# Performance work log

Measured on AMD Instinct MI355X. Metric: run time of the kernel, lower is better.

Reference implementation:

```python
import jax, jax.numpy as jnp
import numpy as np

N_NODES = 100000
N_EDGES = 1600000
IN_DIM = 128
OUT_DIM = 32
NUM_HEADS = 4


def setup_inputs() -> dict:
    key = jax.random.key(0)
    k1, k2, k3, k4, k5, k6 = jax.random.split(key, 6)
    feat = jax.random.normal(k1, (N_NODES, IN_DIM), dtype=jnp.float32)
    # xavier-uniform-ish scales
    fc_w = jax.random.normal(k2, (OUT_DIM * NUM_HEADS, IN_DIM), dtype=jnp.float32) * (1.0 / np.sqrt(IN_DIM))
    attn_src = jax.random.normal(k3, (1, NUM_HEADS, OUT_DIM), dtype=jnp.float32) * 0.1
    attn_dst = jax.random.normal(k4, (1, NUM_HEADS, OUT_DIM), dtype=jnp.float32) * 0.1
    src = jax.random.randint(k5, (N_EDGES,), 0, N_NODES, dtype=jnp.int64)
    dst = jax.random.randint(k6, (N_EDGES,), 0, N_NODES, dtype=jnp.int64)
    return {"feat": feat, "fc_w": fc_w, "attn_src": attn_src, "attn_dst": attn_dst, "src": src, "dst": dst}


def reference(feat, fc_w, attn_src, attn_dst, src, dst):
    N = feat.shape[0]
    # fc: [N, H*D] -> [N, H, D]
    h = (feat @ fc_w.T).reshape(N, NUM_HEADS, OUT_DIM)
    # per-node attention logits [N, H]
    e_src = jnp.sum(h * attn_src, axis=-1)
    e_dst = jnp.sum(h * attn_dst, axis=-1)
    # per-edge logits, LeakyReLU(0.2)  [E, H]
    e = e_src[src] + e_dst[dst]
    e = jnp.where(e > 0, e, 0.2 * e)
    # edge softmax over incoming edges of each dst node
    m = jax.ops.segment_max(e, dst, num_segments=N)          # [N, H], -inf for empty
    a = jnp.exp(e - m[dst])                                  # [E, H]
    s = jax.ops.segment_sum(a, dst, num_segments=N)          # [N, H]
    a = a / jnp.where(s[dst] > 0, s[dst], 1.0)
    # weighted scatter-sum aggregation: u_mul_e + sum
    msg = h[src] * a[:, :, None]                             # [E, H, D]
    out = jax.ops.segment_sum(msg, dst, num_segments=N)      # [N, H, D]
    h_out = out.reshape(N, NUM_HEADS * OUT_DIM)
    # residual: in_dim == out_dim*num_heads -> identity residual
    return h_out + feat
```

## Files before the change

### kernel.cpp

```cpp
#include <hip/hip_runtime.h>

#define HD 128
#define NHEADS 4
#define MBLK 128
#define APITCH 136

#define CHUNK_SHIFT 8
#define MAXCH 512
#define CLCAP 4352
#define PT_EDGES 2048
#define SUB_SHIFT 6
#define SUBN 64
#define CAP 48

#define H8_SCALE   15.875f
#define H8_INVSCALE 0.062992126f

typedef __attribute__((ext_vector_type(8))) short bf16x8;
typedef __attribute__((ext_vector_type(4))) float f32x4;

__device__ __forceinline__ unsigned short f2bf(float x) {
    union { float f; unsigned u; } a; a.f = x;
    unsigned r = a.u + 0x7fffu + ((a.u >> 16) & 1u);
    return (unsigned short)(r >> 16);
}

__global__ __launch_bounds__(256, 2) void gemm_part(
    const float* __restrict__ feat, const float* __restrict__ fc_w,
    const float* __restrict__ attn_src, const float* __restrict__ attn_dst,
    const int* __restrict__ src, const int* __restrict__ dst,
    signed char* __restrict__ h8, float* __restrict__ e_src, float* __restrict__ e_dst,
    int* __restrict__ cursor, unsigned int* __restrict__ clist,
    int2* __restrict__ spillP, int* __restrict__ nspillP,
    int N, int E, int epb, int nchunks, int spillPCap)
{
    __shared__ unsigned short As[MBLK * APITCH];
    __shared__ unsigned short Bs[HD * APITCH];
    const int tid = threadIdx.x;
    const int row0 = blockIdx.x * MBLK;

    {
        int* lcnt = (int*)As;
        int* gbase = lcnt + MAXCH;
        unsigned short* rnk = (unsigned short*)(gbase + MAXCH);
        const int ebase0 = blockIdx.x * epb;
        int eend = ebase0 + epb; if (eend > E) eend = E;
        for (int b0 = ebase0; b0 < eend; b0 += PT_EDGES) {
            int bend = b0 + PT_EDGES; if (bend > eend) bend = eend;
            for (int i = tid; i < MAXCH; i += 256) lcnt[i] = 0;
            __syncthreads();
#pragma unroll
            for (int k = 0; k < PT_EDGES / 256; k++) {
                int idx = tid + k * 256;
                int e = b0 + idx;
                if (e < bend) {
                    int d = dst[e];
                    rnk[idx] = (unsigned short)atomicAdd(&lcnt[d >> CHUNK_SHIFT], 1);
                }
            }
            __syncthreads();
            for (int c = tid; c < nchunks; c += 256) {
                int cnt = lcnt[c];
                gbase[c] = cnt ? atomicAdd(&cursor[c], cnt) : 0;
            }
            __syncthreads();
#pragma unroll
            for (int k = 0; k < PT_EDGES / 256; k++) {
                int idx = tid + k * 256;
                int e = b0 + idx;
                if (e < bend) {
                    int d = dst[e], s = src[e];
                    int c = d >> CHUNK_SHIFT;
                    int pos = gbase[c] + (int)rnk[idx];
                    if (pos < CLCAP && s < (1 << 24)) {
                        clist[(size_t)c * CLCAP + pos] =
                            ((unsigned)(d & (CHUNK_SHIFT == 8 ? 255 : 255)) << 24) | (unsigned)s;
                    } else {
                        int kk = atomicAdd(nspillP, 1);
                        if (kk < spillPCap) spillP[kk] = make_int2(d, s);
                    }
                }
            }
            __syncthreads();
        }
    }
    __syncthreads();

    for (int i = tid; i < 128 * 32; i += 256) {
        int o = i >> 5, j = i & 31;
        float4 v = ((const float4*)fc_w)[i];
        ushort4 u; u.x = f2bf(v.x); u.y = f2bf(v.y); u.z = f2bf(v.z); u.w = f2bf(v.w);
        *(ushort4*)&Bs[o * APITCH + j * 4] = u;
    }
    for (int i = tid; i < MBLK * 32; i += 256) {
        int r = i >> 5, j = i & 31;
        int rowg = row0 + r;
        float4 v = make_float4(0.f, 0.f, 0.f, 0.f);
        if (rowg < N) {
            v = ((const float4*)feat)[(size_t)rowg * 32 + j];
        }
        ushort4 u; u.x = f2bf(v.x); u.y = f2bf(v.y); u.z = f2bf(v.z); u.w = f2bf(v.w);
        *(ushort4*)&As[r * APITCH + j * 4] = u;
    }
    __syncthreads();

    const int w = tid >> 6, lane = tid & 63, quad = lane >> 4, lr = lane & 15;
    f32x4 acc[2][8];
#pragma unroll
    for (int rt = 0; rt < 2; rt++)
#pragma unroll
        for (int ct = 0; ct < 8; ct++) acc[rt][ct] = (f32x4){0.f, 0.f, 0.f, 0.f};

#pragma unroll
    for (int ks = 0; ks < 4; ks++) {
        const int k0 = ks * 32 + quad * 8;
        bf16x8 a0 = *(const bf16x8*)&As[(w * 32 + lr) * APITCH + k0];
        bf16x8 a1 = *(const bf16x8*)&As[(w * 32 + 16 + lr) * APITCH + k0];
        bf16x8 bf[8];
#pragma unroll
        for (int ct = 0; ct < 8; ct++)
            bf[ct] = *(const bf16x8*)&Bs[(ct * 16 + lr) * APITCH + k0];
#pragma unroll
        for (int ct = 0; ct < 8; ct++) {
            acc[0][ct] = __builtin_amdgcn_mfma_f32_16x16x32_bf16(a0, bf[ct], acc[0][ct], 0, 0, 0);
            acc[1][ct] = __builtin_amdgcn_mfma_f32_16x16x32_bf16(a1, bf[ct], acc[1][ct], 0, 0, 0);
        }
    }

#pragma unroll
    for (int rt = 0; rt < 2; rt++) {
#pragma unroll
        for (int ct = 0; ct < 8; ct++) {
            int col = ct * 16 + lr;
#pragma unroll
            for (int reg = 0; reg < 4; reg++) {
                int row = row0 + w * 32 + rt * 16 + quad * 4 + reg;
                if (row < N) {
                    float v = acc[rt][ct][reg];
                    v = fminf(fmaxf(v, -8.f), 8.f);
                    int q = (int)rintf(v * H8_SCALE);
                    h8[(size_t)row * 128 + col] = (signed char)q;
                }
            }
        }
    }

    float as_v[8], ad_v[8];
#pragma unroll
    for (int ct = 0; ct < 8; ct++) {
        as_v[ct] = attn_src[ct * 16 + lr];
        ad_v[ct] = attn_dst[ct * 16 + lr];
    }
#pragma unroll
    for (int rt = 0; rt < 2; rt++) {
#pragma unroll
        for (int reg = 0; reg < 4; reg++) {
            int row = row0 + w * 32 + rt * 16 + quad * 4 + reg;
            float ps[4], pd[4];
#pragma unroll
            for (int hd = 0; hd < 4; hd++) {
                ps[hd] = acc[rt][2 * hd][reg] * as_v[2 * hd] + acc[rt][2 * hd + 1][reg] * as_v[2 * hd + 1];
                pd[hd] = acc[rt][2 * hd][reg] * ad_v[2 * hd] + acc[rt][2 * hd + 1][reg] * ad_v[2 * hd + 1];
            }
#pragma unroll
            for (int off = 1; off < 16; off <<= 1) {
#pragma unroll
                for (int hd = 0; hd < 4; hd++) {
                    ps[hd] += __shfl_xor(ps[hd], off);
                    pd[hd] += __shfl_xor(pd[hd], off);
                }
            }
            if (lr == 0 && row < N) {
                *(float4*)&e_src[(size_t)row * 4] = make_float4(ps[0], ps[1], ps[2], ps[3]);
                *(float4*)&e_dst[(size_t)row * 4] = make_float4(pd[0], pd[1], pd[2], pd[3]);
            }
        }
    }
}

__global__ __launch_bounds__(512) void agg_chunk(
    const unsigned int* __restrict__ clist, const int* __restrict__ cursor,
    const int2* __restrict__ spillP, const int* __restrict__ nspillP,
    const signed char* __restrict__ h8,
    const float* __restrict__ e_src, const float* __restrict__ e_dst,
    const float* __restrict__ feat, float* __restrict__ out,
    int2* __restrict__ spillB, int* __restrict__ nspillB,
    int N, int spillPCap, int spillBCap)
{
    __shared__ int bucket[SUBN][CAP];
    __shared__ int lcnt[SUBN];
    const int c = blockIdx.x;
    const int tid = threadIdx.x;
    const int nodebase = c << SUB_SHIFT;
    const int sub = c & ((1 << (CHUNK_SHIFT - SUB_SHIFT)) - 1);

    if (tid < SUBN) lcnt[tid] = 0;
    __syncthreads();

    const int chunkC = c >> (CHUNK_SHIFT - SUB_SHIFT);
    int cnt = cursor[chunkC]; if (cnt > CLCAP) cnt = CLCAP;
    const unsigned int* base = clist + (size_t)chunkC * CLCAP;
    for (int i = tid; i < cnt; i += 512) {
        unsigned int p = base[i];
        int dl = (int)(p >> 24);
        if ((dl >> SUB_SHIFT) == sub) {
            int ln = dl & (SUBN - 1);
            int pos = atomicAdd(&lcnt[ln], 1);
            if (pos < CAP) bucket[ln][pos] = (int)(p & 0xFFFFFFu);
            else { int kk = atomicAdd(nspillB, 1); if (kk < spillBCap) spillB[kk] = make_int2(nodebase + ln, (int)(p & 0xFFFFFFu)); }
        }
    }
    int nsp = *nspillP; if (nsp > spillPCap) nsp = spillPCap;
    for (int i = tid; i < nsp; i += 512) {
        int2 p = spillP[i];
        if ((p.x >> SUB_SHIFT) == c) {
            int ln = p.x - nodebase;
            int pos = atomicAdd(&lcnt[ln], 1);
            if (pos < CAP) bucket[ln][pos] = p.y;
            else { int kk = atomicAdd(nspillB, 1); if (kk < spillBCap) spillB[kk] = p; }
        }
    }
    __syncthreads();

    const int lane  = tid & 63;
    const int wid   = tid >> 6;
    const int grp8  = lane >> 3;
    const int q     = lane & 7;
    const int head  = q >> 1;

    const int ln = wid * 8 + grp8;
    const int n = nodebase + ln;
    const bool active = (n < N);
    const int deg = active ? lcnt[ln] : 0;
    int md = deg;
    md = max(md, __shfl_xor(md, 8));
    md = max(md, __shfl_xor(md, 16));
    md = max(md, __shfl_xor(md, 32));
    if (md == 0) {
        if (active) {
            const float4* f = (const float4*)(feat + (size_t)n * HD) + q * 4;
            float4* o = (float4*)(out + (size_t)n * HD) + q * 4;
#pragma unroll
            for (int k = 0; k < 4; k++) o[k] = f[k];
        }
        return;
    }
    const float ed = active ? e_dst[(size_t)n * 4 + head] : 0.f;
    const int fdeg = deg < CAP ? deg : CAP;
    const int mdc = md < CAP ? md : CAP;

    f32x4 a0 = (f32x4){0.f, 0.f, 0.f, 0.f};
    f32x4 a1 = (f32x4){0.f, 0.f, 0.f, 0.f};
    f32x4 a2 = (f32x4){0.f, 0.f, 0.f, 0.f};
    f32x4 a3 = (f32x4){0.f, 0.f, 0.f, 0.f};
    float s_l = 0.f;
#pragma unroll 4
    for (int j = 0; j < mdc; ++j) {
        float ev = 0.f; int si = 0;
        if (j < fdeg) {
            si = bucket[ln][j];
            float v = e_src[(size_t)si * 4 + head] + ed;
            v = v > 0.f ? v : 0.2f * v;
            ev = __expf(v);
        }
        s_l += ev;
        const float evs = ev * H8_INVSCALE;
        uint4 hv = *(const uint4*)&h8[(size_t)si * 128 + q * 16];
        a0.x += evs * (float)(int)(signed char)(hv.x);
        a0.y += evs * (float)(int)(signed char)(hv.x >> 8);
        a0.z += evs * (float)(int)(signed char)(hv.x >> 16);
        a0.w += evs * (float)(int)(signed char)(hv.x >> 24);
        a1.x += evs * (float)(int)(signed char)(hv.y);
        a1.y += evs * (float)(int)(signed char)(hv.y >> 8);
        a1.z += evs * (float)(int)(signed char)(hv.y >> 16);
        a1.w += evs * (float)(int)(signed char)(hv.y >> 24);
        a2.x += evs * (float)(int)(signed char)(hv.z);
        a2.y += evs * (float)(int)(signed char)(hv.z >> 8);
        a2.z += evs * (float)(int)(signed char)(hv.z >> 16);
        a2.w += evs * (float)(int)(signed char)(hv.z >> 24);
        a3.x += evs * (float)(int)(signed char)(hv.w);
        a3.y += evs * (float)(int)(signed char)(hv.w >> 8);
        a3.z += evs * (float)(int)(signed char)(hv.w >> 16);
        a3.w += evs * (float)(int)(signed char)(hv.w >> 24);
    }
    if (__any(deg > CAP)) {
        int ns = *nspillB; if (ns > spillBCap) ns = spillBCap;
        for (int k = 0; k < ns; ++k) {
            int2 p = spillB[k];
            if (active && deg > CAP && p.x == n) {
                int si = p.y;
                float v = e_src[(size_t)si * 4 + head] + ed;
                v = v > 0.f ? v : 0.2f * v;
                float ev = __expf(v);
                s_l += ev;
                const float evs = ev * H8_INVSCALE;
                uint4 hv = *(const uint4*)&h8[(size_t)si * 128 + q * 16];
                a0.x += evs * (float)(int)(signed char)(hv.x);
                a0.y += evs * (float)(int)(signed char)(hv.x >> 8);
                a0.z += evs * (float)(int)(signed char)(hv.x >> 16);
                a0.w += evs * (float)(int)(signed char)(hv.x >> 24);
                a1.x += evs * (float)(int)(signed char)(hv.y);
                a1.y += evs * (float)(int)(signed char)(hv.y >> 8);
                a1.z += evs * (float)(int)(signed char)(hv.y >> 16);
                a1.w += evs * (float)(int)(signed char)(hv.y >> 24);
                a2.x += evs * (float)(int)(signed char)(hv.z);
                a2.y += evs * (float)(int)(signed char)(hv.z >> 8);
                a2.z += evs * (float)(int)(signed char)(hv.z >> 16);
                a2.w += evs * (float)(int)(signed char)(hv.z >> 24);
                a3.x += evs * (float)(int)(signed char)(hv.w);
                a3.y += evs * (float)(int)(signed char)(hv.w >> 8);
                a3.z += evs * (float)(int)(signed char)(hv.w >> 16);
                a3.w += evs * (float)(int)(signed char)(hv.w >> 24);
            }
        }
    }
    if (active) {
        const float inv = (deg > 0) ? (1.0f / s_l) : 0.f;
        const float4* f = (const float4*)(feat + (size_t)n * HD) + q * 4;
        float4* o = (float4*)(out + (size_t)n * HD) + q * 4;
        float4 c0 = f[0], c1 = f[1], c2 = f[2], c3 = f[3];
        c0.x += a0.x * inv; c0.y += a0.y * inv; c0.z += a0.z * inv; c0.w += a0.w * inv;
        c1.x += a1.x * inv; c1.y += a1.y * inv; c1.z += a1.z * inv; c1.w += a1.w * inv;
        c2.x += a2.x * inv; c2.y += a2.y * inv; c2.z += a2.z * inv; c2.w += a2.w * inv;
        c3.x += a3.x * inv; c3.y += a3.y * inv; c3.z += a3.z * inv; c3.w += a3.w * inv;
        o[0] = c0; o[1] = c1; o[2] = c2; o[3] = c3;
    }
}

extern "C" void kernel_launch(void* const* d_in, const int* in_sizes, int n_in,
                              void* d_out, int out_size, void* d_ws, size_t ws_size,
                              hipStream_t stream) {
    const float* feat     = (const float*)d_in[0];
    const float* fc_w     = (const float*)d_in[1];
    const float* attn_src = (const float*)d_in[2];
    const float* attn_dst = (const float*)d_in[3];
    const int*   src      = (const int*)d_in[4];
    const int*   dst      = (const int*)d_in[5];
    const int N = in_sizes[0] / HD;
    const int E = in_sizes[4];
    float* out = (float*)d_out;

    const int nchunks = (N + 255) >> CHUNK_SHIFT;
    const int nsub    = (N + SUBN - 1) >> SUB_SHIFT;
    const int spillPCap = E / 8;
    const int spillBCap = E / 8;

    signed char* h8 = (signed char*)d_ws;
    float* e_src  = (float*)(h8 + (size_t)N * HD);
    float* e_dst  = e_src + (size_t)N * NHEADS;
    int* cursor   = (int*)(e_dst + (size_t)N * NHEADS);
    int* nspillP  = cursor + nchunks;
    int* nspillB  = nspillP + 1;
    int hdr = nchunks + 2;
    hdr = (hdr + 1) & ~1;
    unsigned int* clist = (unsigned int*)(cursor + hdr);
    size_t clistLen = (size_t)nchunks * CLCAP;
    clistLen = (clistLen + 1) & ~(size_t)1;
    int2* spillP  = (int2*)(clist + clistLen);
    int2* spillB  = spillP + spillPCap;

    const int G = (N + MBLK - 1) / MBLK;
    const int epb = ((E + G - 1) / G + PT_EDGES - 1) / PT_EDGES * PT_EDGES;

    hipMemsetAsync(cursor, 0, (size_t)(nchunks + 2) * sizeof(int), stream);
    gemm_part<<<G, 256, 0, stream>>>(feat, fc_w, attn_src, attn_dst, src, dst,
                                     h8, e_src, e_dst, cursor, clist, spillP, nspillP,
                                     N, E, epb, nchunks, spillPCap);
    agg_chunk<<<nsub, 512, 0, stream>>>(clist, cursor, spillP, nspillP,
                                        h8, e_src, e_dst, feat, out,
                                        spillB, nspillB, N, spillPCap, spillBCap);
}
```

Measured before the change: 228.6 us.

## Aggregate whole 256-node chunks per block and partition edges into larger slabs

The aggregation kernel now processes an entire 256-node chunk per 1024-thread block, two passes of 128 nodes each. Before, four 64-node sub-blocks each re-read the full chunk edge list and filtered it, so this removes that redundant clist scanning. The edge partition step now hands out fixed 8192-edge slabs in a grid-stride loop instead of per-block ranges, which reduces global cursor atomics per slab. In exchange the aggregation grid shrinks to about 391 large blocks using about 49KB of LDS each, which can lower occupancy and load balance, and the longer slabs lengthen the partition phase inside the GEMM kernel.

```diff
diff --git a/kernel.cpp b/kernel.cpp
--- a/kernel.cpp
+++ b/kernel.cpp
@@ -6,11 +6,10 @@
 #define APITCH 136
 
 #define CHUNK_SHIFT 8
+#define CHUNK_NODES 256
 #define MAXCH 512
 #define CLCAP 4352
-#define PT_EDGES 2048
-#define SUB_SHIFT 6
-#define SUBN 64
+#define PT_EDGES 8192
 #define CAP 48
 
 #define H8_SCALE   15.875f
@@ -32,7 +31,7 @@
     signed char* __restrict__ h8, float* __restrict__ e_src, float* __restrict__ e_dst,
     int* __restrict__ cursor, unsigned int* __restrict__ clist,
     int2* __restrict__ spillP, int* __restrict__ nspillP,
-    int N, int E, int epb, int nchunks, int spillPCap)
+    int N, int E, int npart, int nchunks, int spillPCap)
 {
     __shared__ unsigned short As[MBLK * APITCH];
     __shared__ unsigned short Bs[HD * APITCH];
@@ -43,13 +42,12 @@
         int* lcnt = (int*)As;
         int* gbase = lcnt + MAXCH;
         unsigned short* rnk = (unsigned short*)(gbase + MAXCH);
-        const int ebase0 = blockIdx.x * epb;
-        int eend = ebase0 + epb; if (eend > E) eend = E;
-        for (int b0 = ebase0; b0 < eend; b0 += PT_EDGES) {
-            int bend = b0 + PT_EDGES; if (bend > eend) bend = eend;
+        for (int sb = blockIdx.x; sb < npart; sb += gridDim.x) {
+            const int b0 = sb * PT_EDGES;
+            int bend = b0 + PT_EDGES; if (bend > E) bend = E;
             for (int i = tid; i < MAXCH; i += 256) lcnt[i] = 0;
             __syncthreads();
-#pragma unroll
+#pragma unroll 4
             for (int k = 0; k < PT_EDGES / 256; k++) {
                 int idx = tid + k * 256;
                 int e = b0 + idx;
@@ -64,7 +62,7 @@
                 gbase[c] = cnt ? atomicAdd(&cursor[c], cnt) : 0;
             }
             __syncthreads();
-#pragma unroll
+#pragma unroll 4
             for (int k = 0; k < PT_EDGES / 256; k++) {
                 int idx = tid + k * 256;
                 int e = b0 + idx;
@@ -73,8 +71,7 @@
                     int c = d >> CHUNK_SHIFT;
                     int pos = gbase[c] + (int)rnk[idx];
                     if (pos < CLCAP && s < (1 << 24)) {
-                        clist[(size_t)c * CLCAP + pos] =
-                            ((unsigned)(d & (CHUNK_SHIFT == 8 ? 255 : 255)) << 24) | (unsigned)s;
+                        clist[(size_t)c * CLCAP + pos] = ((unsigned)(d & 255) << 24) | (unsigned)s;
                     } else {
                         int kk = atomicAdd(nspillP, 1);
                         if (kk < spillPCap) spillP[kk] = make_int2(d, s);
@@ -178,7 +175,7 @@
     }
 }
 
-__global__ __launch_bounds__(512) void agg_chunk(
+__global__ __launch_bounds__(1024) void agg_chunk(
     const unsigned int* __restrict__ clist, const int* __restrict__ cursor,
     const int2* __restrict__ spillP, const int* __restrict__ nspillP,
     const signed char* __restrict__ h8,
@@ -187,33 +184,28 @@
     int2* __restrict__ spillB, int* __restrict__ nspillB,
     int N, int spillPCap, int spillBCap)
 {
-    __shared__ int bucket[SUBN][CAP];
-    __shared__ int lcnt[SUBN];
+    __shared__ int bucket[CHUNK_NODES][CAP];
+    __shared__ int lcnt[CHUNK_NODES];
     const int c = blockIdx.x;
     const int tid = threadIdx.x;
-    const int nodebase = c << SUB_SHIFT;
-    const int sub = c & ((1 << (CHUNK_SHIFT - SUB_SHIFT)) - 1);
-
-    if (tid < SUBN) lcnt[tid] = 0;
+    const int nodebase = c << CHUNK_SHIFT;
+
+    if (tid < CHUNK_NODES) lcnt[tid] = 0;
     __syncthreads();
 
-    const int chunkC = c >> (CHUNK_SHIFT - SUB_SHIFT);
-    int cnt = cursor[chunkC]; if (cnt > CLCAP) cnt = CLCAP;
-    const unsigned int* base = clist + (size_t)chunkC * CLCAP;
-    for (int i = tid; i < cnt; i += 512) {
+    int cnt = cursor[c]; if (cnt > CLCAP) cnt = CLCAP;
+    const unsigned int* base = clist + (size_t)c * CLCAP;
+    for (int i = tid; i < cnt; i += 1024) {
         unsigned int p = base[i];
-        int dl = (int)(p >> 24);
-        if ((dl >> SUB_SHIFT) == sub) {
-            int ln = dl & (SUBN - 1);
-            int pos = atomicAdd(&lcnt[ln], 1);
-            if (pos < CAP) bucket[ln][pos] = (int)(p & 0xFFFFFFu);
-            else { int kk = atomicAdd(nspillB, 1); if (kk < spillBCap) spillB[kk] = make_int2(nodebase + ln, (int)(p & 0xFFFFFFu)); }
-        }
+        int ln = (int)(p >> 24);
+        int pos = atomicAdd(&lcnt[ln], 1);
+        if (pos < CAP) bucket[ln][pos] = (int)(p & 0xFFFFFFu);
+        else { int kk = atomicAdd(nspillB, 1); if (kk < spillBCap) spillB[kk] = make_int2(nodebase + ln, (int)(p & 0xFFFFFFu)); }
     }
     int nsp = *nspillP; if (nsp > spillPCap) nsp = spillPCap;
-    for (int i = tid; i < nsp; i += 512) {
+    for (int i = tid; i < nsp; i += 1024) {
         int2 p = spillP[i];
-        if ((p.x >> SUB_SHIFT) == c) {
+        if ((p.x >> CHUNK_SHIFT) == c) {
             int ln = p.x - nodebase;
             int pos = atomicAdd(&lcnt[ln], 1);
             if (pos < CAP) bucket[ln][pos] = p.y;
@@ -228,102 +220,105 @@
     const int q     = lane & 7;
     const int head  = q >> 1;
 
-    const int ln = wid * 8 + grp8;
-    const int n = nodebase + ln;
-    const bool active = (n < N);
-    const int deg = active ? lcnt[ln] : 0;
-    int md = deg;
-    md = max(md, __shfl_xor(md, 8));
-    md = max(md, __shfl_xor(md, 16));
-    md = max(md, __shfl_xor(md, 32));
-    if (md == 0) {
+#pragma unroll
+    for (int pass = 0; pass < 2; pass++) {
+        const int ln = pass * 128 + wid * 8 + grp8;
+        const int n = nodebase + ln;
+        const bool active = (n < N);
+        const int deg = active ? lcnt[ln] : 0;
+        int md = deg;
+        md = max(md, __shfl_xor(md, 8));
+        md = max(md, __shfl_xor(md, 16));
+        md = max(md, __shfl_xor(md, 32));
+        if (md == 0) {
+            if (active) {
+                const float4* f = (const float4*)(feat + (size_t)n * HD) + q * 4;
+                float4* o = (float4*)(out + (size_t)n * HD) + q * 4;
+#pragma unroll
+                for (int k = 0; k < 4; k++) o[k] = f[k];
+            }
+            continue;
+        }
+        const float ed = active ? e_dst[(size_t)n * 4 + head] : 0.f;
+        const int fdeg = deg < CAP ? deg : CAP;
+        const int mdc = md < CAP ? md : CAP;
+
+        f32x4 a0 = (f32x4){0.f, 0.f, 0.f, 0.f};
+        f32x4 a1 = (f32x4){0.f, 0.f, 0.f, 0.f};
+        f32x4 a2 = (f32x4){0.f, 0.f, 0.f, 0.f};
+        f32x4 a3 = (f32x4){0.f, 0.f, 0.f, 0.f};
+        float s_l = 0.f;
+#pragma unroll 4
+        for (int j = 0; j < mdc; ++j) {
+            float ev = 0.f; int si = 0;
+            if (j < fdeg) {
+                si = bucket[ln][j];
+                float v = e_src[(size_t)si * 4 + head] + ed;
+                v = v > 0.f ? v : 0.2f * v;
+                ev = __expf(v);
+            }
+            s_l += ev;
+            const float evs = ev * H8_INVSCALE;
+            uint4 hv = *(const uint4*)&h8[(size_t)si * 128 + q * 16];
+            a0.x += evs * (float)(int)(signed char)(hv.x);
+            a0.y += evs * (float)(int)(signed char)(hv.x >> 8);
+            a0.z += evs * (float)(int)(signed char)(hv.x >> 16);
+            a0.w += evs * (float)(int)(signed char)(hv.x >> 24);
+            a1.x += evs * (float)(int)(signed char)(hv.y);
+            a1.y += evs * (float)(int)(signed char)(hv.y >> 8);
+            a1.z += evs * (float)(int)(signed char)(hv.y >> 16);
+            a1.w += evs * (float)(int)(signed char)(hv.y >> 24);
+            a2.x += evs * (float)(int)(signed char)(hv.z);
+            a2.y += evs * (float)(int)(signed char)(hv.z >> 8);
+            a2.z += evs * (float)(int)(signed char)(hv.z >> 16);
+            a2.w += evs * (float)(int)(signed char)(hv.z >> 24);
+            a3.x += evs * (float)(int)(signed char)(hv.w);
+            a3.y += evs * (float)(int)(signed char)(hv.w >> 8);
+            a3.z += evs * (float)(int)(signed char)(hv.w >> 16);
+            a3.w += evs * (float)(int)(signed char)(hv.w >> 24);
+        }
+        if (__any(deg > CAP)) {
+            int ns = *nspillB; if (ns > spillBCap) ns = spillBCap;
+            for (int k = 0; k < ns; ++k) {
+                int2 p = spillB[k];
+                if (active && deg > CAP && p.x == n) {
+                    int si = p.y;
+                    float v = e_src[(size_t)si * 4 + head] + ed;
+                    v = v > 0.f ? v : 0.2f * v;
+                    float ev = __expf(v);
+                    s_l += ev;
+                    const float evs = ev * H8_INVSCALE;
+                    uint4 hv = *(const uint4*)&h8[(size_t)si * 128 + q * 16];
+                    a0.x += evs * (float)(int)(signed char)(hv.x);
+                    a0.y += evs * (float)(int)(signed char)(hv.x >> 8);
+                    a0.z += evs * (float)(int)(signed char)(hv.x >> 16);
+                    a0.w += evs * (float)(int)(signed char)(hv.x >> 24);
+                    a1.x += evs * (float)(int)(signed char)(hv.y);
+                    a1.y += evs * (float)(int)(signed char)(hv.y >> 8);
+                    a1.z += evs * (float)(int)(signed char)(hv.y >> 16);
+                    a1.w += evs * (float)(int)(signed char)(hv.y >> 24);
+                    a2.x += evs * (float)(int)(signed char)(hv.z);
+                    a2.y += evs * (float)(int)(signed char)(hv.z >> 8);
+                    a2.z += evs * (float)(int)(signed char)(hv.z >> 16);
+                    a2.w += evs * (float)(int)(signed char)(hv.z >> 24);
+                    a3.x += evs * (float)(int)(signed char)(hv.w);
+                    a3.y += evs * (float)(int)(signed char)(hv.w >> 8);
+                    a3.z += evs * (float)(int)(signed char)(hv.w >> 16);
+                    a3.w += evs * (float)(int)(signed char)(hv.w >> 24);
+                }
+            }
+        }
         if (active) {
+            const float inv = (deg > 0) ? (1.0f / s_l) : 0.f;
             const float4* f = (const float4*)(feat + (size_t)n * HD) + q * 4;
             float4* o = (float4*)(out + (size_t)n * HD) + q * 4;
-#pragma unroll
-            for (int k = 0; k < 4; k++) o[k] = f[k];
-        }
-        return;
-    }
-    const float ed = active ? e_dst[(size_t)n * 4 + head] : 0.f;
-    const int fdeg = deg < CAP ? deg : CAP;
-    const int mdc = md < CAP ? md : CAP;
-
-    f32x4 a0 = (f32x4){0.f, 0.f, 0.f, 0.f};
-    f32x4 a1 = (f32x4){0.f, 0.f, 0.f, 0.f};
-    f32x4 a2 = (f32x4){0.f, 0.f, 0.f, 0.f};
-    f32x4 a3 = (f32x4){0.f, 0.f, 0.f, 0.f};
-    float s_l = 0.f;
-#pragma unroll 4
-    for (int j = 0; j < mdc; ++j) {
-        float ev = 0.f; int si = 0;
-        if (j < fdeg) {
-            si = bucket[ln][j];
-            float v = e_src[(size_t)si * 4 + head] + ed;
-            v = v > 0.f ? v : 0.2f * v;
-            ev = __expf(v);
-        }
-        s_l += ev;
-        const float evs = ev * H8_INVSCALE;
-        uint4 hv = *(const uint4*)&h8[(size_t)si * 128 + q * 16];
-        a0.x += evs * (float)(int)(signed char)(hv.x);
-        a0.y += evs * (float)(int)(signed char)(hv.x >> 8);
-        a0.z += evs * (float)(int)(signed char)(hv.x >> 16);
-        a0.w += evs * (float)(int)(signed char)(hv.x >> 24);
-        a1.x += evs * (float)(int)(signed char)(hv.y);
-        a1.y += evs * (float)(int)(signed char)(hv.y >> 8);
-        a1.z += evs * (float)(int)(signed char)(hv.y >> 16);
-        a1.w += evs * (float)(int)(signed char)(hv.y >> 24);
-        a2.x += evs * (float)(int)(signed char)(hv.z);
-        a2.y += evs * (float)(int)(signed char)(hv.z >> 8);
-        a2.z += evs * (float)(int)(signed char)(hv.z >> 16);
-        a2.w += evs * (float)(int)(signed char)(hv.z >> 24);
-        a3.x += evs * (float)(int)(signed char)(hv.w);
-        a3.y += evs * (float)(int)(signed char)(hv.w >> 8);
-        a3.z += evs * (float)(int)(signed char)(hv.w >> 16);
-        a3.w += evs * (float)(int)(signed char)(hv.w >> 24);
-    }
-    if (__any(deg > CAP)) {
-        int ns = *nspillB; if (ns > spillBCap) ns = spillBCap;
-        for (int k = 0; k < ns; ++k) {
-            int2 p = spillB[k];
-            if (active && deg > CAP && p.x == n) {
-                int si = p.y;
-                float v = e_src[(size_t)si * 4 + head] + ed;
-                v = v > 0.f ? v : 0.2f * v;
-                float ev = __expf(v);
-                s_l += ev;
-                const float evs = ev * H8_INVSCALE;
-                uint4 hv = *(const uint4*)&h8[(size_t)si * 128 + q * 16];
-                a0.x += evs * (float)(int)(signed char)(hv.x);
-                a0.y += evs * (float)(int)(signed char)(hv.x >> 8);
-                a0.z += evs * (float)(int)(signed char)(hv.x >> 16);
-                a0.w += evs * (float)(int)(signed char)(hv.x >> 24);
-                a1.x += evs * (float)(int)(signed char)(hv.y);
-                a1.y += evs * (float)(int)(signed char)(hv.y >> 8);
-                a1.z += evs * (float)(int)(signed char)(hv.y >> 16);
-                a1.w += evs * (float)(int)(signed char)(hv.y >> 24);
-                a2.x += evs * (float)(int)(signed char)(hv.z);
-                a2.y += evs * (float)(int)(signed char)(hv.z >> 8);
-                a2.z += evs * (float)(int)(signed char)(hv.z >> 16);
-                a2.w += evs * (float)(int)(signed char)(hv.z >> 24);
-                a3.x += evs * (float)(int)(signed char)(hv.w);
-                a3.y += evs * (float)(int)(signed char)(hv.w >> 8);
-                a3.z += evs * (float)(int)(signed char)(hv.w >> 16);
-                a3.w += evs * (float)(int)(signed char)(hv.w >> 24);
-            }
-        }
-    }
-    if (active) {
-        const float inv = (deg > 0) ? (1.0f / s_l) : 0.f;
-        const float4* f = (const float4*)(feat + (size_t)n * HD) + q * 4;
-        float4* o = (float4*)(out + (size_t)n * HD) + q * 4;
-        float4 c0 = f[0], c1 = f[1], c2 = f[2], c3 = f[3];
-        c0.x += a0.x * inv; c0.y += a0.y * inv; c0.z += a0.z * inv; c0.w += a0.w * inv;
-        c1.x += a1.x * inv; c1.y += a1.y * inv; c1.z += a1.z * inv; c1.w += a1.w * inv;
-        c2.x += a2.x * inv; c2.y += a2.y * inv; c2.z += a2.z * inv; c2.w += a2.w * inv;
-        c3.x += a3.x * inv; c3.y += a3.y * inv; c3.z += a3.z * inv; c3.w += a3.w * inv;
-        o[0] = c0; o[1] = c1; o[2] = c2; o[3] = c3;
+            float4 c0 = f[0], c1 = f[1], c2 = f[2], c3 = f[3];
+            c0.x += a0.x * inv; c0.y += a0.y * inv; c0.z += a0.z * inv; c0.w += a0.w * inv;
+            c1.x += a1.x * inv; c1.y += a1.y * inv; c1.z += a1.z * inv; c1.w += a1.w * inv;
+            c2.x += a2.x * inv; c2.y += a2.y * inv; c2.z += a2.z * inv; c2.w += a2.w * inv;
+            c3.x += a3.x * inv; c3.y += a3.y * inv; c3.z += a3.z * inv; c3.w += a3.w * inv;
+            o[0] = c0; o[1] = c1; o[2] = c2; o[3] = c3;
+        }
     }
 }
 
@@ -340,8 +335,7 @@
     const int E = in_sizes[4];
     float* out = (float*)d_out;
 
-    const int nchunks = (N + 255) >> CHUNK_SHIFT;
-    const int nsub    = (N + SUBN - 1) >> SUB_SHIFT;
+    const int nchunks = (N + CHUNK_NODES - 1) >> CHUNK_SHIFT;
     const int spillPCap = E / 8;
     const int spillBCap = E / 8;
 
@@ -360,13 +354,13 @@
     int2* spillB  = spillP + spillPCap;
 
     const int G = (N + MBLK - 1) / MBLK;
-    const int epb = ((E + G - 1) / G + PT_EDGES - 1) / PT_EDGES * PT_EDGES;
+    const int npart = (E + PT_EDGES - 1) / PT_EDGES;
 
     hipMemsetAsync(cursor, 0, (size_t)(nchunks + 2) * sizeof(int), stream);
     gemm_part<<<G, 256, 0, stream>>>(feat, fc_w, attn_src, attn_dst, src, dst,
                                      h8, e_src, e_dst, cursor, clist, spillP, nspillP,
-                                     N, E, epb, nchunks, spillPCap);
-    agg_chunk<<<nsub, 512, 0, stream>>>(clist, cursor, spillP, nspillP,
-                                        h8, e_src, e_dst, feat, out,
-                                        spillB, nspillB, N, spillPCap, spillBCap);
+                                     N, E, npart, nchunks, spillPCap);
+    agg_chunk<<<nchunks, 1024, 0, stream>>>(clist, cursor, spillP, nspillP,
+                                            h8, e_src, e_dst, feat, out,
+                                            spillB, nspillB, N, spillPCap, spillBCap);
 }
```

Result: no change. 229.8 us (+0.5%).
